# Kernel tuning notes

Hardware: AMD Instinct MI355X
Metric: run time of the kernel (lower is better)

## Reference

```python
import jax, jax.numpy as jnp
import numpy as np

D_MODEL = 2048
D_INNER = 4096            # expand * d_model
D_XB = 1024
D_STATE = 128
HEADDIM = 64
NHEADS = D_INNER // HEADDIM            # 64
NGROUPS = D_INNER // D_STATE           # 32 (d_inner == ngroups * d_state)
HPG = NHEADS // NGROUPS                # heads per B/C group = 2
REPEAT = D_INNER // D_XB               # repeat_kv factor = 4
XB_GROUPS = D_XB // D_STATE            # 8
CHUNK = 256
D_CONV = 4
CONV_DIM = D_INNER + 2 * D_XB          # 6144
D_IN_PROJ = D_INNER + 2 * D_XB + D_INNER + NHEADS  # 10304 -> d_mlp = 0
NORM_GS = D_INNER // NGROUPS           # gated group-RMSNorm group size = 128
EPS = 1e-5


def setup_inputs() -> dict:
    key = jax.random.key(0)
    ks = jax.random.split(key, 8)
    u = jax.random.normal(ks[0], (2, 2048, D_MODEL), jnp.float32)
    W_in = jax.random.normal(ks[1], (D_IN_PROJ, D_MODEL), jnp.float32) * 0.02
    conv_w = jax.random.normal(ks[2], (CONV_DIM, D_CONV), jnp.float32) * 0.2
    conv_b = jnp.zeros((CONV_DIM,), jnp.float32)
    # dt_bias = inverse-softplus of dt ~ LogUniform(dt_min, dt_max), as in __init__
    dt = jnp.exp(jax.random.uniform(ks[3], (NHEADS,), jnp.float32)
                 * (np.log(0.1) - np.log(0.001)) + np.log(0.001))
    dt_bias = dt + jnp.log(-jnp.expm1(-dt))
    A_log = jnp.log(jax.random.uniform(ks[4], (NHEADS,), jnp.float32, minval=1.0, maxval=16.0))
    D = jnp.ones((NHEADS,), jnp.float32)
    norm_weight = jnp.ones((D_INNER,), jnp.float32)
    W_out = jax.random.normal(ks[5], (D_MODEL, D_INNER), jnp.float32) * 0.02
    return dict(u=u, W_in=W_in, conv_w=conv_w, conv_b=conv_b, dt_bias=dt_bias,
                A_log=A_log, D=D, norm_weight=norm_weight, W_out=W_out)


def _segsum(x):
    # x: (..., T); out[..., t, s] = sum_{s < i <= t} x_i for s <= t else -inf
    T = x.shape[-1]
    cs = jnp.cumsum(x, axis=-1)
    seg = cs[..., :, None] - cs[..., None, :]
    mask = jnp.tril(jnp.ones((T, T), bool))
    return jnp.where(mask, seg, -jnp.inf)


def _chunked_scan(x, dt, A, Bh, Ch, D):
    # SSD chunked selective scan (mamba_chunk_scan_combined math).
    # x: (b,l,h,p), dt: (b,l,h) post-softplus, A: (h,), Bh/Ch: (b,l,h,n), D: (h,)
    b, l, h, p = x.shape
    c = l // CHUNK
    xc = x.reshape(b, c, CHUNK, h, p)
    dtc = dt.reshape(b, c, CHUNK, h)
    Bc = Bh.reshape(b, c, CHUNK, h, D_STATE)
    Cc = Ch.reshape(b, c, CHUNK, h, D_STATE)
    dA = jnp.transpose(dtc * A, (0, 3, 1, 2))          # (b,h,c,cl)
    dA_cs = jnp.cumsum(dA, axis=-1)                     # (b,h,c,cl)
    L = jnp.exp(_segsum(dA))                            # (b,h,c,cl,cl), lower-tri decay
    xdt = xc * dtc[..., None]                           # (b,c,cl,h,p)
    # intra-chunk (diagonal block) output
    G = jnp.einsum('bclhn,bcshn->bhcls', Cc, Bc)
    Y_diag = jnp.einsum('bhcls,bcshp->bclhp', G * L, xdt)
    # per-chunk final states
    decay_states = jnp.exp(dA_cs[..., -1:] - dA_cs)     # (b,h,c,cl)
    states = jnp.einsum('bcshn,bhcs,bcshp->bchpn', Bc, decay_states, xdt)
    # inter-chunk recurrence
    chunk_decay = jnp.exp(dA_cs[..., -1])               # (b,h,c)
    states_t = jnp.moveaxis(states, 1, 0)               # (c,b,h,p,n)
    decay_t = jnp.moveaxis(chunk_decay, -1, 0)          # (c,b,h)
    def step(carry, inp):
        s, d = inp
        return carry * d[..., None, None] + s, carry
    _, prev = jax.lax.scan(step, jnp.zeros_like(states_t[0]), (states_t, decay_t))
    prev = jnp.moveaxis(prev, 0, 1)                     # (b,c,h,p,n) state entering each chunk
    Y_off = jnp.einsum('bclhn,bchpn,bhcl->bclhp', Cc, prev, jnp.exp(dA_cs))
    y = Y_diag + Y_off + xc * D[:, None]                # D skip uses raw x
    return y.reshape(b, l, h, p)


def reference(u, W_in, conv_w, conv_b, dt_bias, A_log, D, norm_weight, W_out):
    b, l, _ = u.shape
    zxbcdt = u @ W_in.T                                 # (b,l,10304); d_mlp == 0
    z, xBC, dt = jnp.split(zxbcdt, [D_INNER, D_INNER + CONV_DIM], axis=-1)
    # causal depthwise conv1d (kernel D_CONV) + SiLU (causal_conv1d_fn semantics)
    xp = jnp.pad(xBC, ((0, 0), (D_CONV - 1, 0), (0, 0)))
    conv = conv_b
    for k in range(D_CONV):
        conv = conv + xp[:, k:k + l, :] * conv_w[:, k]
    xBC = jax.nn.silu(conv)
    x, B, C = jnp.split(xBC, [D_XB, 2 * D_XB], axis=-1)
    # GQA-style repeat_kv (repeat_interleave over d_state-sized groups)
    x = jnp.repeat(x.reshape(b, l, XB_GROUPS, D_STATE), REPEAT, axis=2).reshape(b, l, D_INNER)
    B = jnp.repeat(B.reshape(b, l, XB_GROUPS, D_STATE), REPEAT, axis=2)   # (b,l,NGROUPS,n)
    C = C.reshape(b, l, NGROUPS, D_STATE)
    # broadcast groups to heads (head h uses group h // HPG)
    Bh = jnp.repeat(B, HPG, axis=2)
    Ch = jnp.repeat(C, HPG, axis=2)
    xh = x.reshape(b, l, NHEADS, HEADDIM)
    dt = jax.nn.softplus(dt + dt_bias)                  # dt_softplus=True
    A = -jnp.exp(A_log)
    y = _chunked_scan(xh, dt, A, Bh, Ch, D).reshape(b, l, D_INNER)
    # RMSNormGated (norm_before_gate=False): gate then grouped RMSNorm
    y = y * jax.nn.silu(z)
    yg = y.reshape(b, l, NGROUPS, NORM_GS)
    rstd = jax.lax.rsqrt(jnp.mean(yg * yg, axis=-1, keepdims=True) + EPS)
    y = (yg * rstd).reshape(b, l, D_INNER) * norm_weight
    return y @ W_out.T
```

## Files before the change

### kernel.cpp

```cpp
#include <hip/hip_runtime.h>
#include <cstdint>
#include <cstddef>

typedef unsigned int uint;
typedef unsigned short ushort;

typedef __bf16 bf16x8 __attribute__((ext_vector_type(8)));
typedef float f32x4 __attribute__((ext_vector_type(4)));

__device__ __forceinline__ float bflo(uint u) { return __uint_as_float(u << 16); }
__device__ __forceinline__ float bfhi(uint u) { return __uint_as_float(u & 0xffff0000u); }
__device__ __forceinline__ float bf2f(ushort s) { return __uint_as_float(((uint)s) << 16); }
__device__ __forceinline__ ushort f2bf(float f) {
    uint u = __float_as_uint(f);
    u += 0x7fffu + ((u >> 16) & 1u);
    return (ushort)(u >> 16);
}
__device__ __forceinline__ uint pk2(float lo, float hi) {
    return (uint)f2bf(lo) | ((uint)f2bf(hi) << 16);
}
__device__ __forceinline__ void unpack8(uint4 v, float* f) {
    f[0] = bflo(v.x); f[1] = bfhi(v.x); f[2] = bflo(v.y); f[3] = bfhi(v.y);
    f[4] = bflo(v.z); f[5] = bfhi(v.z); f[6] = bflo(v.w); f[7] = bfhi(v.w);
}

typedef __attribute__((address_space(1))) const unsigned int* as1_cuptr;
typedef __attribute__((address_space(3))) unsigned int* as3_uptr;
__device__ __forceinline__ void gload_lds16(const void* g, void* l) {
    __builtin_amdgcn_global_load_lds((as1_cuptr)g, (as3_uptr)l, 16, 0, 0);
}

#define LTOT 4096
#define DMODEL 2048
#define DINNER 4096
#define DSTATE 128
#define NHEADS 64
#define CONVDIM 6144
#define DPROJ 10304
#define CHUNK 256
#define NCHUNK 16

__global__ void cvt_kernel(const float* __restrict__ in, ushort* __restrict__ out, int n4) {
    int i = blockIdx.x * 256 + threadIdx.x;
    if (i < n4) {
        float4 v = ((const float4*)in)[i];
        ushort4 o;
        o.x = f2bf(v.x); o.y = f2bf(v.y); o.z = f2bf(v.z); o.w = f2bf(v.w);
        ((ushort4*)out)[i] = o;
    }
}

#define MFMA_OP __builtin_amdgcn_mfma_f32_16x16x32_bf16
#define MM16(MB) do { \
  acc[(MB)+0][0]=MFMA_OP(a0,b0,acc[(MB)+0][0],0,0,0); acc[(MB)+0][1]=MFMA_OP(a0,b1,acc[(MB)+0][1],0,0,0); \
  acc[(MB)+0][2]=MFMA_OP(a0,b2,acc[(MB)+0][2],0,0,0); acc[(MB)+0][3]=MFMA_OP(a0,b3,acc[(MB)+0][3],0,0,0); \
  acc[(MB)+1][0]=MFMA_OP(a1,b0,acc[(MB)+1][0],0,0,0); acc[(MB)+1][1]=MFMA_OP(a1,b1,acc[(MB)+1][1],0,0,0); \
  acc[(MB)+1][2]=MFMA_OP(a1,b2,acc[(MB)+1][2],0,0,0); acc[(MB)+1][3]=MFMA_OP(a1,b3,acc[(MB)+1][3],0,0,0); \
  acc[(MB)+2][0]=MFMA_OP(a2,b0,acc[(MB)+2][0],0,0,0); acc[(MB)+2][1]=MFMA_OP(a2,b1,acc[(MB)+2][1],0,0,0); \
  acc[(MB)+2][2]=MFMA_OP(a2,b2,acc[(MB)+2][2],0,0,0); acc[(MB)+2][3]=MFMA_OP(a2,b3,acc[(MB)+2][3],0,0,0); \
  acc[(MB)+3][0]=MFMA_OP(a3,b0,acc[(MB)+3][0],0,0,0); acc[(MB)+3][1]=MFMA_OP(a3,b1,acc[(MB)+3][1],0,0,0); \
  acc[(MB)+3][2]=MFMA_OP(a3,b2,acc[(MB)+3][2],0,0,0); acc[(MB)+3][3]=MFMA_OP(a3,b3,acc[(MB)+3][3],0,0,0); \
} while (0)

#define RD8(BASE, OFF) (*(const bf16x8*)((BASE) + (OFF)))

__global__ __launch_bounds__(512, 2) void gemm256_in(
    const ushort* __restrict__ X, const ushort* __restrict__ W,
    ushort* __restrict__ zbuf, ushort* __restrict__ xbc, float* __restrict__ dtraw) {
    __shared__ ushort AL[2][16384];
    __shared__ ushort BL[2][16384];
    const int NBN = 41;
    int q = gridDim.x >> 3;
    int wg = blockIdx.x;
    int swz = (wg & 7) * q + (wg >> 3);
    int per = NBN * 4;
    int sg = swz / per, rr = swz % per;
    int bm = sg * 4 + (rr & 3);
    int bn = rr >> 2;
    int tid = threadIdx.x;
    int lane = tid & 63, w = tid >> 6;
    int wr = w >> 2, wc = w & 3;
    int lr = lane & 15, g = lane >> 4;
    int y00 = ((lr >> 1) << 7) | ((lr & 1) << 6) | (g << 4);
    int z00 = y00 ^ (((y00 >> 7) & 7) << 4);
    int aBase = wr * 8192 + z00;
    int bBase = wc * 4096 + z00;
    int z0 = tid * 16, z1 = z0 + 8192;
    int y0 = z0 ^ (((z0 >> 7) & 7) << 4);
    int y1 = z1 ^ (((z1 >> 7) & 7) << 4);
    int row0s = ((y0 >> 7) << 1) | ((y0 >> 6) & 1), kbe0 = (y0 & 63) >> 1;
    int row1s = ((y1 >> 7) << 1) | ((y1 >> 6) & 1), kbe1 = (y1 & 63) >> 1;
    const ushort* gA0 = &X[(size_t)(bm * 256 + row0s) * 2048 + kbe0];
    const ushort* gA1 = &X[(size_t)(bm * 256 + row1s) * 2048 + kbe1];
    const ushort* gB0 = &W[(size_t)(bn * 256 + row0s) * 2048 + kbe0];
    const ushort* gB1 = &W[(size_t)(bn * 256 + row1s) * 2048 + kbe1];
    int wOff = w * 1024;

#define STAGE(DB, ARR, KP, P0, P1, KO) do { \
    gload_lds16((P0) + (KO) + (KP) * 32, (char*)(ARR) + (DB) * 32768 + (KP) * 16384 + wOff); \
    gload_lds16((P1) + (KO) + (KP) * 32, (char*)(ARR) + (DB) * 32768 + (KP) * 16384 + wOff + 8192); \
} while (0)

    f32x4 acc[8][4] = {};
    STAGE(0, AL, 0, gA0, gA1, 0);
    STAGE(0, BL, 0, gB0, gB1, 0);
    STAGE(0, AL, 1, gA0, gA1, 0);
    STAGE(0, BL, 1, gB0, gB1, 0);

    for (int t = 0; t < 32; ++t) {
        int buf = t & 1, nb = buf ^ 1;
        int ko = ((t + 1) & 31) * 64;
        const char* Ab = (const char*)AL + buf * 32768;
        const char* Bb = (const char*)BL + buf * 32768;
        bf16x8 a0, a1, a2, a3, b0, b1, b2, b3;
        asm volatile("s_waitcnt vmcnt(4)" ::: "memory");
        __builtin_amdgcn_s_barrier();
        __builtin_amdgcn_sched_barrier(0);
        b0 = RD8(Bb, bBase);        b1 = RD8(Bb, bBase + 1024);
        b2 = RD8(Bb, bBase + 2048); b3 = RD8(Bb, bBase + 3072);
        a0 = RD8(Ab, aBase);        a1 = RD8(Ab, aBase + 1024);
        a2 = RD8(Ab, aBase + 2048); a3 = RD8(Ab, aBase + 3072);
        STAGE(nb, AL, 0, gA0, gA1, ko);
        __builtin_amdgcn_s_setprio(1);
        MM16(0);
        __builtin_amdgcn_s_setprio(0);
        __builtin_amdgcn_sched_barrier(0);
        __builtin_amdgcn_s_barrier();
        __builtin_amdgcn_sched_barrier(0);
        a0 = RD8(Ab, aBase + 4096);        a1 = RD8(Ab, aBase + 4096 + 1024);
        a2 = RD8(Ab, aBase + 4096 + 2048); a3 = RD8(Ab, aBase + 4096 + 3072);
        STAGE(nb, BL, 0, gB0, gB1, ko);
        __builtin_amdgcn_s_setprio(1);
        MM16(4);
        __builtin_amdgcn_s_setprio(0);
        asm volatile("s_waitcnt vmcnt(4)" ::: "memory");
        __builtin_amdgcn_s_barrier();
        __builtin_amdgcn_sched_barrier(0);
        b0 = RD8(Bb, bBase + 16384);        b1 = RD8(Bb, bBase + 16384 + 1024);
        b2 = RD8(Bb, bBase + 16384 + 2048); b3 = RD8(Bb, bBase + 16384 + 3072);
        a0 = RD8(Ab, aBase + 16384);        a1 = RD8(Ab, aBase + 16384 + 1024);
        a2 = RD8(Ab, aBase + 16384 + 2048); a3 = RD8(Ab, aBase + 16384 + 3072);
        STAGE(nb, AL, 1, gA0, gA1, ko);
        __builtin_amdgcn_s_setprio(1);
        MM16(0);
        __builtin_amdgcn_s_setprio(0);
        __builtin_amdgcn_sched_barrier(0);
        __builtin_amdgcn_s_barrier();
        __builtin_amdgcn_sched_barrier(0);
        a0 = RD8(Ab, aBase + 16384 + 4096);        a1 = RD8(Ab, aBase + 16384 + 4096 + 1024);
        a2 = RD8(Ab, aBase + 16384 + 4096 + 2048); a3 = RD8(Ab, aBase + 16384 + 4096 + 3072);
        STAGE(nb, BL, 1, gB0, gB1, ko);
        __builtin_amdgcn_s_setprio(1);
        MM16(4);
        __builtin_amdgcn_s_setprio(0);
    }
    asm volatile("s_waitcnt vmcnt(0)" ::: "memory");

    int rq = g * 4;
    #pragma unroll
    for (int mf = 0; mf < 8; mf++) {
        int row0 = bm * 256 + wr * 128 + mf * 16 + rq;
        #pragma unroll
        for (int n = 0; n < 4; n++) {
            int cb0 = bn * 256 + wc * 64 + n * 16;
            int col = cb0 + lr;
            if (cb0 < 4096) {
                #pragma unroll
                for (int r = 0; r < 4; r++)
                    zbuf[(size_t)(row0 + r) * DINNER + col] = f2bf(acc[mf][n][r]);
            } else if (cb0 < 10240) {
                #pragma unroll
                for (int r = 0; r < 4; r++)
                    xbc[(size_t)(row0 + r) * CONVDIM + (col - 4096)] = f2bf(acc[mf][n][r]);
            } else if (cb0 < 10304) {
                #pragma unroll
                for (int r = 0; r < 4; r++)
                    dtraw[(size_t)(row0 + r) * 64 + (col - 10240)] = acc[mf][n][r];
            }
        }
    }
}
#undef STAGE

__global__ __launch_bounds__(512, 2) void gemm256_out(
    const ushort* __restrict__ X, const ushort* __restrict__ W,
    float* __restrict__ outF) {
    __shared__ ushort AL[2][16384];
    __shared__ ushort BL[2][8192];
    int q = gridDim.x >> 3;
    int wg = blockIdx.x;
    int swz = (wg & 7) * q + (wg >> 3);
    int per = 16 * 4;
    int sg = swz / per, rr = swz % per;
    int bm = sg * 4 + (rr & 3);
    int bn = rr >> 2;
    int tid = threadIdx.x;
    int lane = tid & 63, w = tid >> 6;
    int wr = w >> 1, wc = w & 1;
    int lr = lane & 15, g = lane >> 4;
    int y00 = ((lr >> 1) << 7) | ((lr & 1) << 6) | (g << 4);
    int z00 = y00 ^ (((y00 >> 7) & 7) << 4);
    int aBase = wr * 4096 + z00;
    int bBase = wc * 4096 + z00;
    int z0 = tid * 16, z1 = z0 + 8192;
    int y0 = z0 ^ (((z0 >> 7) & 7) << 4);
    int y1 = z1 ^ (((z1 >> 7) & 7) << 4);
    int rowA0 = ((y0 >> 7) << 1) | ((y0 >> 6) & 1), kA0 = (y0 & 63) >> 1;
    int rowA1 = ((y1 >> 7) << 1) | ((y1 >> 6) & 1), kA1 = (y1 & 63) >> 1;
    const ushort* gA0 = &X[(size_t)(bm * 256 + rowA0) * 4096 + kA0];
    const ushort* gA1 = &X[(size_t)(bm * 256 + rowA1) * 4096 + kA1];
    const ushort* gB  = &W[(size_t)(bn * 128 + rowA0) * 4096 + kA0];
    int wOff = w * 1024;

#define STAGEA(DB, KP, KO) do { \
    gload_lds16(gA0 + (KO) + (KP) * 32, (char*)AL + (DB) * 32768 + (KP) * 16384 + wOff); \
    gload_lds16(gA1 + (KO) + (KP) * 32, (char*)AL + (DB) * 32768 + (KP) * 16384 + wOff + 8192); \
} while (0)
#define STAGEB(DB, KP, KO) \
    gload_lds16(gB + (KO) + (KP) * 32, (char*)BL + (DB) * 16384 + (KP) * 8192 + wOff)

    f32x4 acc[4][4] = {};
    STAGEA(0, 0, 0); STAGEB(0, 0, 0);
    STAGEA(0, 1, 0); STAGEB(0, 1, 0);

    for (int t = 0; t < 64; ++t) {
        int buf = t & 1, nb = buf ^ 1;
        int ko = ((t + 1) & 63) * 64;
        const char* Ab = (const char*)AL + buf * 32768;
        const char* Bb = (const char*)BL + buf * 16384;
        bf16x8 a0, a1, a2, a3, b0, b1, b2, b3;
        asm volatile("s_waitcnt vmcnt(3)" ::: "memory");
        __builtin_amdgcn_s_barrier();
        __builtin_amdgcn_sched_barrier(0);
        b0 = RD8(Bb, bBase);        b1 = RD8(Bb, bBase + 1024);
        b2 = RD8(Bb, bBase + 2048); b3 = RD8(Bb, bBase + 3072);
        a0 = RD8(Ab, aBase);        a1 = RD8(Ab, aBase + 1024);
        a2 = RD8(Ab, aBase + 2048); a3 = RD8(Ab, aBase + 3072);
        STAGEA(nb, 0, ko); STAGEB(nb, 0, ko);
        __builtin_amdgcn_s_setprio(1);
        MM16(0);
        __builtin_amdgcn_s_setprio(0);
        __builtin_amdgcn_sched_barrier(0);
        asm volatile("s_waitcnt vmcnt(3)" ::: "memory");
        __builtin_amdgcn_s_barrier();
        __builtin_amdgcn_sched_barrier(0);
        b0 = RD8(Bb, bBase + 8192);        b1 = RD8(Bb, bBase + 8192 + 1024);
        b2 = RD8(Bb, bBase + 8192 + 2048); b3 = RD8(Bb, bBase + 8192 + 3072);
        a0 = RD8(Ab, aBase + 16384);        a1 = RD8(Ab, aBase + 16384 + 1024);
        a2 = RD8(Ab, aBase + 16384 + 2048); a3 = RD8(Ab, aBase + 16384 + 3072);
        STAGEA(nb, 1, ko); STAGEB(nb, 1, ko);
        __builtin_amdgcn_s_setprio(1);
        MM16(0);
        __builtin_amdgcn_s_setprio(0);
        __builtin_amdgcn_sched_barrier(0);
    }
    asm volatile("s_waitcnt vmcnt(0)" ::: "memory");

    int rq = g * 4;
    #pragma unroll
    for (int mf = 0; mf < 4; mf++) {
        int row0 = bm * 256 + wr * 64 + mf * 16 + rq;
        #pragma unroll
        for (int nf = 0; nf < 4; nf++) {
            int col = bn * 128 + wc * 64 + nf * 16 + lr;
            #pragma unroll
            for (int r = 0; r < 4; r++)
                outF[(size_t)(row0 + r) * DMODEL + col] = acc[mf][nf][r];
        }
    }
}
#undef STAGEA
#undef STAGEB

__global__ void conv_kernel(const ushort* __restrict__ xbc, const float* __restrict__ cw,
                            const float* __restrict__ cb, ushort* __restrict__ convout) {
    int c8 = (blockIdx.x * 256 + threadIdx.x) * 8;
    int row0 = blockIdx.y * 4;
    int t0 = row0 & 2047;
    float bias[8];
    {
        float4 b0 = ((const float4*)cb)[c8 / 4];
        float4 b1 = ((const float4*)cb)[c8 / 4 + 1];
        bias[0] = b0.x; bias[1] = b0.y; bias[2] = b0.z; bias[3] = b0.w;
        bias[4] = b1.x; bias[5] = b1.y; bias[6] = b1.z; bias[7] = b1.w;
    }
    float wk[8][4];
    #pragma unroll
    for (int e = 0; e < 8; e++) {
        float4 wv = ((const float4*)cw)[c8 + e];
        wk[e][0] = wv.x; wk[e][1] = wv.y; wk[e][2] = wv.z; wk[e][3] = wv.w;
    }
    float f[7][8];
    #pragma unroll
    for (int j = 0; j < 7; j++) {
        int tt = t0 - 3 + j;
        if (tt >= 0) {
            uint4 v = *(const uint4*)&xbc[(size_t)(row0 - 3 + j) * CONVDIM + c8];
            unpack8(v, f[j]);
        } else {
            #pragma unroll
            for (int e = 0; e < 8; e++) f[j][e] = 0.f;
        }
    }
    #pragma unroll
    for (int r = 0; r < 4; r++) {
        float a[8];
        #pragma unroll
        for (int e = 0; e < 8; e++) {
            a[e] = bias[e];
            #pragma unroll
            for (int k = 0; k < 4; k++) a[e] += f[r + k][e] * wk[e][k];
        }
        uint4 o;
        float s[8];
        #pragma unroll
        for (int e = 0; e < 8; e++) s[e] = a[e] / (1.f + __expf(-a[e]));
        o.x = pk2(s[0], s[1]); o.y = pk2(s[2], s[3]);
        o.z = pk2(s[4], s[5]); o.w = pk2(s[6], s[7]);
        *(uint4*)&convout[(size_t)(row0 + r) * CONVDIM + c8] = o;
    }
}

__global__ void cumsum_kernel(float* __restrict__ dtbuf, const float* __restrict__ dt_bias,
                              const float* __restrict__ A_log, float* __restrict__ dAcs) {
    int bi = blockIdx.x;
    int h = bi & 63, cg = bi >> 6;
    int t = threadIdx.x;
    size_t didx = (size_t)(cg * 256 + t) * 64 + h;
    float x = dtbuf[didx] + dt_bias[h];
    float sp = (x > 20.f) ? x : log1pf(__expf(x));
    dtbuf[didx] = sp;
    float A = -expf(A_log[h]);
    float v = sp * A;
    __shared__ float s[256];
    s[t] = v;
    __syncthreads();
    for (int off = 1; off < 256; off <<= 1) {
        float add = (t >= off) ? s[t - off] : 0.f;
        __syncthreads();
        s[t] += add;
        __syncthreads();
    }
    dAcs[(size_t)bi * 256 + t] = s[t];
}

__global__ __launch_bounds__(256) void states_mfma(
    const ushort* __restrict__ convout, const float* __restrict__ dtsp,
    const float* __restrict__ dAcs, float* __restrict__ states) {
    __shared__ ushort BT[128 * 72];
    __shared__ ushort XT[64 * 72];
    int bi = blockIdx.x;
    int h = bi & 63, cg = bi >> 6;
    int tid = threadIdx.x;
    int rowbase = cg * 256;
    int bcol = 1024 + ((h >> 3) << 7);
    int xcol = ((h >> 3) << 7) + ((h & 1) << 6);
    float dAlast = dAcs[(size_t)bi * 256 + 255];
    int w = tid >> 6, lane = tid & 63, g = lane >> 4, cc = lane & 15;
    f32x4 acc[4][2] = {};
    for (int T = 0; T < 4; T++) {
        __syncthreads();
        int s = lane;
        int srow = rowbase + T * 64 + s;
        #pragma unroll
        for (int i = 0; i < 4; i++) {
            int n0 = (w + i * 4) * 8;
            uint4 v = *(const uint4*)&convout[(size_t)srow * CONVDIM + bcol + n0];
            ushort us[8];
            us[0] = (ushort)v.x; us[1] = (ushort)(v.x >> 16);
            us[2] = (ushort)v.y; us[3] = (ushort)(v.y >> 16);
            us[4] = (ushort)v.z; us[5] = (ushort)(v.z >> 16);
            us[6] = (ushort)v.w; us[7] = (ushort)(v.w >> 16);
            #pragma unroll
            for (int e = 0; e < 8; e++) BT[(n0 + e) * 72 + s] = us[e];
        }
        float wgt = dtsp[(size_t)srow * 64 + h] * __expf(dAlast - dAcs[(size_t)bi * 256 + T * 64 + s]);
        #pragma unroll
        for (int j = 0; j < 2; j++) {
            int p0 = (w * 2 + j) * 8;
            uint4 v = *(const uint4*)&convout[(size_t)srow * CONVDIM + xcol + p0];
            float f[8]; unpack8(v, f);
            #pragma unroll
            for (int e = 0; e < 8; e++) XT[(p0 + e) * 72 + s] = f2bf(f[e] * wgt);
        }
        __syncthreads();
        bf16x8 af[4][2], bw[2][2];
        #pragma unroll
        for (int m = 0; m < 4; m++)
            #pragma unroll
            for (int kb = 0; kb < 2; kb++)
                af[m][kb] = *(const bf16x8*)&XT[(m * 16 + cc) * 72 + kb * 32 + 8 * g];
        #pragma unroll
        for (int np = 0; np < 2; np++)
            #pragma unroll
            for (int kb = 0; kb < 2; kb++)
                bw[np][kb] = *(const bf16x8*)&BT[(w * 32 + np * 16 + cc) * 72 + kb * 32 + 8 * g];
        #pragma unroll
        for (int m = 0; m < 4; m++)
            #pragma unroll
            for (int np = 0; np < 2; np++) {
                acc[m][np] = MFMA_OP(af[m][0], bw[np][0], acc[m][np], 0, 0, 0);
                acc[m][np] = MFMA_OP(af[m][1], bw[np][1], acc[m][np], 0, 0, 0);
            }
    }
    size_t base = (size_t)bi * 8192;
    #pragma unroll
    for (int m = 0; m < 4; m++)
        #pragma unroll
        for (int np = 0; np < 2; np++)
            #pragma unroll
            for (int r = 0; r < 4; r++) {
                int p = m * 16 + 4 * g + r;
                int n = w * 32 + np * 16 + cc;
                states[base + (size_t)p * 128 + n] = acc[m][np][r];
            }
}

__global__ void recur_kernel(const float* __restrict__ dAcs, float* __restrict__ states) {
    int blk = blockIdx.x;
    int pq = blk & 7, bh = blk >> 3;
    int h = bh & 63, b = bh >> 6;
    int tid = threadIdx.x;
    int p = pq * 8 + (tid >> 5);
    int n0 = (tid & 31) * 4;
    float4 carry = make_float4(0.f, 0.f, 0.f, 0.f);
    for (int c = 0; c < 8; c++) {
        int bi = (b * 8 + c) * 64 + h;
        float decay = __expf(dAcs[(size_t)bi * 256 + 255]);
        size_t idx = (size_t)bi * 8192 + (size_t)p * 128 + n0;
        float4 tmp = *(const float4*)&states[idx];
        *(float4*)&states[idx] = carry;
        carry.x = carry.x * decay + tmp.x;
        carry.y = carry.y * decay + tmp.y;
        carry.z = carry.z * decay + tmp.z;
        carry.w = carry.w * decay + tmp.w;
    }
}

__global__ __launch_bounds__(256, 2) void yscan_mfma(
    const ushort* __restrict__ convout, const float* __restrict__ dtsp,
    const float* __restrict__ dAcs, const float* __restrict__ states,
    ushort* __restrict__ y) {
    __shared__ ushort XT[64 * 264];
    __shared__ ushort PR[64 * 136];
    __shared__ ushort PV[4 * 16 * 72];
    __shared__ float sdA[256];
    int bi = blockIdx.x;
    int h = bi & 63, cg = bi >> 6;
    int tid = threadIdx.x;
    int rowbase = cg * 256;
    int bcol = 1024 + ((h >> 3) << 7);
    int ccol = 2048 + ((h >> 1) << 7);
    int xcol = ((h >> 3) << 7) + ((h & 1) << 6);

    sdA[tid] = dAcs[(size_t)bi * 256 + tid];
    #pragma unroll
    for (int i = 0; i < 4; i++) {
        int s = i * 64 + (tid & 63);
        float dtv = dtsp[(size_t)(rowbase + s) * 64 + h];
        #pragma unroll
        for (int j = 0; j < 2; j++) {
            int p0 = (((tid >> 6) << 1) + j) << 3;
            uint4 v = *(const uint4*)&convout[(size_t)(rowbase + s) * CONVDIM + xcol + p0];
            float f[8]; unpack8(v, f);
            #pragma unroll
            for (int e = 0; e < 8; e++) XT[(p0 + e) * 264 + s] = f2bf(f[e] * dtv);
        }
    }
    {
        const float* pv = &states[(size_t)bi * 8192];
        #pragma unroll
        for (int i = 0; i < 8; i++) {
            int flat = i * 1024 + tid * 4;
            float4 v = *(const float4*)&pv[flat];
            int p = flat >> 7, n = flat & 127;
            *(uint*)&PR[p * 136 + n]     = pk2(v.x, v.y);
            *(uint*)&PR[p * 136 + n + 2] = pk2(v.z, v.w);
        }
    }
    __syncthreads();

    int w = tid >> 6, lane = tid & 63, g = lane >> 4, c = lane & 15;
    int wbase = w * 64;
    const ushort* Crow0 = &convout[(size_t)(rowbase + wbase + c) * CONVDIM + ccol + 8 * g];

    f32x4 yac[4][4] = {};
    #pragma unroll
    for (int kb = 0; kb < 4; kb++) {
        bf16x8 pb[4];
        #pragma unroll
        for (int np = 0; np < 4; np++)
            pb[np] = *(const bf16x8*)&PR[(16 * np + c) * 136 + kb * 32 + 8 * g];
        #pragma unroll
        for (int m = 0; m < 4; m++) {
            bf16x8 cf = *(const bf16x8*)&Crow0[(size_t)(m * 16) * CONVDIM + kb * 32];
            #pragma unroll
            for (int np = 0; np < 4; np++)
                yac[m][np] = MFMA_OP(cf, pb[np], yac[m][np], 0, 0, 0);
        }
    }
    float al[4][4];
    float Sw = sdA[wbase];
    float eSw = __expf(Sw);
    #pragma unroll
    for (int m = 0; m < 4; m++)
        #pragma unroll
        for (int r = 0; r < 4; r++) {
            float dAl = sdA[wbase + m * 16 + 4 * g + r];
            al[m][r] = __expf(dAl - Sw);
            float el = al[m][r] * eSw;
            #pragma unroll
            for (int np = 0; np < 4; np++) yac[m][np][r] *= el;
        }

    ushort* pvs = &PV[w * 1152];
    for (int T = 0; T <= w; T++) {
        f32x4 sac[4][4] = {};
        #pragma unroll
        for (int kb = 0; kb < 4; kb++) {
            bf16x8 bb[4];
            #pragma unroll
            for (int np = 0; np < 4; np++)
                bb[np] = *(const bf16x8*)&convout[(size_t)(rowbase + T * 64 + 16 * np + c) * CONVDIM + bcol + kb * 32 + 8 * g];
            #pragma unroll
            for (int m = 0; m < 4; m++) {
                bf16x8 cf = *(const bf16x8*)&Crow0[(size_t)(m * 16) * CONVDIM + kb * 32];
                #pragma unroll
                for (int np = 0; np < 4; np++)
                    sac[m][np] = MFMA_OP(cf, bb[np], sac[m][np], 0, 0, 0);
            }
        }
        bf16x8 xb[4][2];
        #pragma unroll
        for (int np = 0; np < 4; np++)
            #pragma unroll
            for (int k2 = 0; k2 < 2; k2++)
                xb[np][k2] = *(const bf16x8*)&XT[(16 * np + c) * 264 + T * 64 + k2 * 32 + 8 * g];
        if (T < w) {
            float ET = sdA[T * 64 + 63];
            float cT = __expf(Sw - ET);
            float bc[4];
            #pragma unroll
            for (int np = 0; np < 4; np++)
                bc[np] = __expf(ET - sdA[T * 64 + 16 * np + c]) * cT;
            #pragma unroll
            for (int m = 0; m < 4; m++) {
                #pragma unroll
                for (int np = 0; np < 4; np++) {
                    float s0 = bc[np];
                    #pragma unroll
                    for (int r = 0; r < 4; r++)
                        pvs[(4 * g + r) * 72 + 16 * np + c] = f2bf(sac[m][np][r] * (al[m][r] * s0));
                }
                bf16x8 pa0 = *(const bf16x8*)&pvs[c * 72 + 8 * g];
                bf16x8 pa1 = *(const bf16x8*)&pvs[c * 72 + 32 + 8 * g];
                #pragma unroll
                for (int np = 0; np < 4; np++) {
                    yac[m][np] = MFMA_OP(pa0, xb[np][0], yac[m][np], 0, 0, 0);
                    yac[m][np] = MFMA_OP(pa1, xb[np][1], yac[m][np], 0, 0, 0);
                }
            }
        } else {
            #pragma unroll
            for (int m = 0; m < 4; m++) {
                float dal[4];
                #pragma unroll
                for (int r = 0; r < 4; r++) dal[r] = sdA[wbase + m * 16 + 4 * g + r];
                #pragma unroll
                for (int np = 0; np < 4; np++) {
                    int s_loc = w * 64 + 16 * np + c;
                    float dAs = sdA[s_loc];
                    #pragma unroll
                    for (int r = 0; r < 4; r++) {
                        int l_loc = wbase + m * 16 + 4 * g + r;
                        float v = (s_loc <= l_loc) ? sac[m][np][r] * __expf(dal[r] - dAs) : 0.f;
                        pvs[(4 * g + r) * 72 + 16 * np + c] = f2bf(v);
                    }
                }
                bf16x8 pa0 = *(const bf16x8*)&pvs[c * 72 + 8 * g];
                bf16x8 pa1 = *(const bf16x8*)&pvs[c * 72 + 32 + 8 * g];
                #pragma unroll
                for (int np = 0; np < 4; np++) {
                    yac[m][np] = MFMA_OP(pa0, xb[np][0], yac[m][np], 0, 0, 0);
                    yac[m][np] = MFMA_OP(pa1, xb[np][1], yac[m][np], 0, 0, 0);
                }
            }
        }
    }
    #pragma unroll
    for (int m = 0; m < 4; m++)
        #pragma unroll
        for (int np = 0; np < 4; np++)
            #pragma unroll
            for (int r = 0; r < 4; r++) {
                int l = wbase + m * 16 + 4 * g + r;
                y[(size_t)(rowbase + l) * DINNER + h * 64 + 16 * np + c] = f2bf(yac[m][np][r]);
            }
}

__global__ void norm_kernel(ushort* __restrict__ y, const ushort* __restrict__ zbuf,
                            const ushort* __restrict__ convout, const float* __restrict__ Dvec,
                            const float* __restrict__ nw) {
    int row = blockIdx.x;
    int g = blockIdx.y * 4 + (threadIdx.x >> 6);
    int lane = threadIdx.x & 63;
    int cbase = g * 128 + lane * 2;
    int h = cbase >> 6;
    int p = cbase & 63;
    int xc = ((h >> 3) << 7) + ((h & 1) << 6) + p;
    uint yv = *(const uint*)&y[(size_t)row * DINNER + cbase];
    uint zv = *(const uint*)&zbuf[(size_t)row * DINNER + cbase];
    uint xv = *(const uint*)&convout[(size_t)row * CONVDIM + xc];
    float Dh = Dvec[h];
    float y0 = bflo(yv) + Dh * bflo(xv), y1 = bfhi(yv) + Dh * bfhi(xv);
    float z0 = bflo(zv), z1 = bfhi(zv);
    float v0 = y0 * (z0 / (1.f + __expf(-z0)));
    float v1 = y1 * (z1 / (1.f + __expf(-z1)));
    float ss = v0 * v0 + v1 * v1;
    #pragma unroll
    for (int off = 32; off; off >>= 1) ss += __shfl_xor(ss, off, 64);
    float rstd = rsqrtf(ss * (1.f / 128.f) + 1e-5f);
    v0 *= rstd * nw[cbase];
    v1 *= rstd * nw[cbase + 1];
    *(uint*)&y[(size_t)row * DINNER + cbase] = pk2(v0, v1);
}

extern "C" void kernel_launch(void* const* d_in, const int* in_sizes, int n_in,
                              void* d_out, int out_size, void* d_ws, size_t ws_size,
                              hipStream_t stream) {
    const float* u       = (const float*)d_in[0];
    const float* W_in    = (const float*)d_in[1];
    const float* conv_w  = (const float*)d_in[2];
    const float* conv_b  = (const float*)d_in[3];
    const float* dt_bias = (const float*)d_in[4];
    const float* A_log   = (const float*)d_in[5];
    const float* Dvec    = (const float*)d_in[6];
    const float* nw      = (const float*)d_in[7];
    const float* W_out   = (const float*)d_in[8];

    char* ws = (char*)d_ws;
    size_t off = 0;
    auto alloc = [&](size_t bytes) { void* p = ws + off; off += (bytes + 255) & ~(size_t)255; return p; };
    ushort* zbuf    = (ushort*)alloc((size_t)LTOT * DINNER * 2);
    void*   shreg   = alloc((size_t)LTOT * CONVDIM * 2);
    ushort* xbc     = (ushort*)shreg;
    float*  states  = (float*)shreg;
    ushort* Wout_bf = (ushort*)shreg;
    float*  dtbuf   = (float*) alloc((size_t)LTOT * 64 * 4);
    void*   convreg = alloc((size_t)LTOT * CONVDIM * 2);
    ushort* Win_bf  = (ushort*)convreg;
    ushort* convout = (ushort*)convreg;
    float*  dAcs    = (float*) alloc((size_t)1024 * 256 * 4);
    void*   ybreg   = alloc((size_t)LTOT * DINNER * 2);
    ushort* u_bf    = (ushort*)ybreg;
    ushort* ybuf    = (ushort*)ybreg;

    cvt_kernel<<<dim3(8192),  dim3(256), 0, stream>>>(u, u_bf, 2097152);
    cvt_kernel<<<dim3(20608), dim3(256), 0, stream>>>(W_in, Win_bf, 5275648);
    gemm256_in<<<dim3(656), dim3(512), 0, stream>>>(u_bf, Win_bf, zbuf, xbc, dtbuf);
    conv_kernel<<<dim3(3, 1024), dim3(256), 0, stream>>>(xbc, conv_w, conv_b, convout);
    cumsum_kernel<<<dim3(1024), dim3(256), 0, stream>>>(dtbuf, dt_bias, A_log, dAcs);
    states_mfma<<<dim3(1024), dim3(256), 0, stream>>>(convout, dtbuf, dAcs, states);
    recur_kernel<<<dim3(1024), dim3(256), 0, stream>>>(dAcs, states);
    yscan_mfma<<<dim3(1024), dim3(256), 0, stream>>>(convout, dtbuf, dAcs, states, ybuf);
    cvt_kernel<<<dim3(8192), dim3(256), 0, stream>>>(W_out, Wout_bf, 2097152);
    norm_kernel<<<dim3(4096, 8), dim3(256), 0, stream>>>(ybuf, zbuf, convout, Dvec, nw);
    gemm256_out<<<dim3(256), dim3(512), 0, stream>>>(ybuf, Wout_bf, (float*)d_out);
}
```

Baseline: 498.7 us.

## Software-pipeline LDS fragment reads in input-projection GEMM across MFMA phases

Restructures the in-projection GEMM main loop so each phase's LDS fragment loads for the next phase are issued before the current phase's MFMAs run. The fragments are kept in separate register arrays, and the first k-half of the next buffer is prefetched at the end of each iteration. This cuts the number of barriers per iteration from four to two and retunes the vmcnt waits, aiming to hide LDS latency behind matrix math. The cost is more live vector registers, which could cause spills under the 2-block occupancy bound, plus subtler synchronization correctness around buffer reuse.

```diff
diff --git a/kernel.cpp b/kernel.cpp
--- a/kernel.cpp
+++ b/kernel.cpp
@@ -51,15 +51,12 @@
 }
 
 #define MFMA_OP __builtin_amdgcn_mfma_f32_16x16x32_bf16
-#define MM16(MB) do { \
-  acc[(MB)+0][0]=MFMA_OP(a0,b0,acc[(MB)+0][0],0,0,0); acc[(MB)+0][1]=MFMA_OP(a0,b1,acc[(MB)+0][1],0,0,0); \
-  acc[(MB)+0][2]=MFMA_OP(a0,b2,acc[(MB)+0][2],0,0,0); acc[(MB)+0][3]=MFMA_OP(a0,b3,acc[(MB)+0][3],0,0,0); \
-  acc[(MB)+1][0]=MFMA_OP(a1,b0,acc[(MB)+1][0],0,0,0); acc[(MB)+1][1]=MFMA_OP(a1,b1,acc[(MB)+1][1],0,0,0); \
-  acc[(MB)+1][2]=MFMA_OP(a1,b2,acc[(MB)+1][2],0,0,0); acc[(MB)+1][3]=MFMA_OP(a1,b3,acc[(MB)+1][3],0,0,0); \
-  acc[(MB)+2][0]=MFMA_OP(a2,b0,acc[(MB)+2][0],0,0,0); acc[(MB)+2][1]=MFMA_OP(a2,b1,acc[(MB)+2][1],0,0,0); \
-  acc[(MB)+2][2]=MFMA_OP(a2,b2,acc[(MB)+2][2],0,0,0); acc[(MB)+2][3]=MFMA_OP(a2,b3,acc[(MB)+2][3],0,0,0); \
-  acc[(MB)+3][0]=MFMA_OP(a3,b0,acc[(MB)+3][0],0,0,0); acc[(MB)+3][1]=MFMA_OP(a3,b1,acc[(MB)+3][1],0,0,0); \
-  acc[(MB)+3][2]=MFMA_OP(a3,b2,acc[(MB)+3][2],0,0,0); acc[(MB)+3][3]=MFMA_OP(a3,b3,acc[(MB)+3][3],0,0,0); \
+#define MMX(MB, AV, BV) do { \
+  _Pragma("unroll") \
+  for (int _m = 0; _m < 4; _m++) \
+    _Pragma("unroll") \
+    for (int _n = 0; _n < 4; _n++) \
+      acc[(MB)+_m][_n] = MFMA_OP(AV[_m], BV[_n], acc[(MB)+_m][_n], 0, 0, 0); \
 } while (0)
 
 #define RD8(BASE, OFF) (*(const bf16x8*)((BASE) + (OFF)))
@@ -102,57 +99,71 @@
 } while (0)
 
     f32x4 acc[8][4] = {};
+    bf16x8 bLo[4], bHi[4], aE[4], aO[4];
     STAGE(0, AL, 0, gA0, gA1, 0);
     STAGE(0, BL, 0, gB0, gB1, 0);
     STAGE(0, AL, 1, gA0, gA1, 0);
     STAGE(0, BL, 1, gB0, gB1, 0);
+    asm volatile("s_waitcnt vmcnt(4)" ::: "memory");
+    __builtin_amdgcn_s_barrier();
+    __builtin_amdgcn_sched_barrier(0);
+    {
+        const char* Ab = (const char*)AL;
+        const char* Bb = (const char*)BL;
+        #pragma unroll
+        for (int i = 0; i < 4; i++) {
+            bLo[i] = RD8(Bb, bBase + i * 1024);
+            aE[i]  = RD8(Ab, aBase + i * 1024);
+        }
+    }
 
     for (int t = 0; t < 32; ++t) {
         int buf = t & 1, nb = buf ^ 1;
         int ko = ((t + 1) & 31) * 64;
-        const char* Ab = (const char*)AL + buf * 32768;
-        const char* Bb = (const char*)BL + buf * 32768;
-        bf16x8 a0, a1, a2, a3, b0, b1, b2, b3;
-        asm volatile("s_waitcnt vmcnt(4)" ::: "memory");
-        __builtin_amdgcn_s_barrier();
-        __builtin_amdgcn_sched_barrier(0);
-        b0 = RD8(Bb, bBase);        b1 = RD8(Bb, bBase + 1024);
-        b2 = RD8(Bb, bBase + 2048); b3 = RD8(Bb, bBase + 3072);
-        a0 = RD8(Ab, aBase);        a1 = RD8(Ab, aBase + 1024);
-        a2 = RD8(Ab, aBase + 2048); a3 = RD8(Ab, aBase + 3072);
+        const char* Ab  = (const char*)AL + buf * 32768;
+        const char* Bb  = (const char*)BL + buf * 32768;
+        const char* AbN = (const char*)AL + nb * 32768;
+        const char* BbN = (const char*)BL + nb * 32768;
+        #pragma unroll
+        for (int i = 0; i < 4; i++) aO[i] = RD8(Ab, aBase + 4096 + i * 1024);
         STAGE(nb, AL, 0, gA0, gA1, ko);
         __builtin_amdgcn_s_setprio(1);
-        MM16(0);
+        MMX(0, aE, bLo);
         __builtin_amdgcn_s_setprio(0);
         __builtin_amdgcn_sched_barrier(0);
+        asm volatile("s_waitcnt vmcnt(2)" ::: "memory");
         __builtin_amdgcn_s_barrier();
         __builtin_amdgcn_sched_barrier(0);
-        a0 = RD8(Ab, aBase + 4096);        a1 = RD8(Ab, aBase + 4096 + 1024);
-        a2 = RD8(Ab, aBase + 4096 + 2048); a3 = RD8(Ab, aBase + 4096 + 3072);
+        #pragma unroll
+        for (int i = 0; i < 4; i++) {
+            bHi[i] = RD8(Bb, bBase + 16384 + i * 1024);
+            aE[i]  = RD8(Ab, aBase + 16384 + i * 1024);
+        }
         STAGE(nb, BL, 0, gB0, gB1, ko);
         __builtin_amdgcn_s_setprio(1);
-        MM16(4);
+        MMX(4, aO, bLo);
         __builtin_amdgcn_s_setprio(0);
-        asm volatile("s_waitcnt vmcnt(4)" ::: "memory");
-        __builtin_amdgcn_s_barrier();
-        __builtin_amdgcn_sched_barrier(0);
-        b0 = RD8(Bb, bBase + 16384);        b1 = RD8(Bb, bBase + 16384 + 1024);
-        b2 = RD8(Bb, bBase + 16384 + 2048); b3 = RD8(Bb, bBase + 16384 + 3072);
-        a0 = RD8(Ab, aBase + 16384);        a1 = RD8(Ab, aBase + 16384 + 1024);
-        a2 = RD8(Ab, aBase + 16384 + 2048); a3 = RD8(Ab, aBase + 16384 + 3072);
+        __builtin_amdgcn_sched_barrier(0);
+        #pragma unroll
+        for (int i = 0; i < 4; i++) aO[i] = RD8(Ab, aBase + 16384 + 4096 + i * 1024);
         STAGE(nb, AL, 1, gA0, gA1, ko);
         __builtin_amdgcn_s_setprio(1);
-        MM16(0);
+        MMX(0, aE, bHi);
         __builtin_amdgcn_s_setprio(0);
         __builtin_amdgcn_sched_barrier(0);
+        asm volatile("s_waitcnt vmcnt(2)" ::: "memory");
         __builtin_amdgcn_s_barrier();
         __builtin_amdgcn_sched_barrier(0);
-        a0 = RD8(Ab, aBase + 16384 + 4096);        a1 = RD8(Ab, aBase + 16384 + 4096 + 1024);
-        a2 = RD8(Ab, aBase + 16384 + 4096 + 2048); a3 = RD8(Ab, aBase + 16384 + 4096 + 3072);
+        #pragma unroll
+        for (int i = 0; i < 4; i++) {
+            bLo[i] = RD8(BbN, bBase + i * 1024);
+            aE[i]  = RD8(AbN, aBase + i * 1024);
+        }
         STAGE(nb, BL, 1, gB0, gB1, ko);
         __builtin_amdgcn_s_setprio(1);
-        MM16(4);
+        MMX(4, aO, bHi);
         __builtin_amdgcn_s_setprio(0);
+        __builtin_amdgcn_sched_barrier(0);
     }
     asm volatile("s_waitcnt vmcnt(0)" ::: "memory");
 
@@ -181,6 +192,17 @@
     }
 }
 #undef STAGE
+
+#define MM16(MB) do { \
+  acc[(MB)+0][0]=MFMA_OP(a0,b0,acc[(MB)+0][0],0,0,0); acc[(MB)+0][1]=MFMA_OP(a0,b1,acc[(MB)+0][1],0,0,0); \
+  acc[(MB)+0][2]=MFMA_OP(a0,b2,acc[(MB)+0][2],0,0,0); acc[(MB)+0][3]=MFMA_OP(a0,b3,acc[(MB)+0][3],0,0,0); \
+  acc[(MB)+1][0]=MFMA_OP(a1,b0,acc[(MB)+1][0],0,0,0); acc[(MB)+1][1]=MFMA_OP(a1,b1,acc[(MB)+1][1],0,0,0); \
+  acc[(MB)+1][2]=MFMA_OP(a1,b2,acc[(MB)+1][2],0,0,0); acc[(MB)+1][3]=MFMA_OP(a1,b3,acc[(MB)+1][3],0,0,0); \
+  acc[(MB)+2][0]=MFMA_OP(a2,b0,acc[(MB)+2][0],0,0,0); acc[(MB)+2][1]=MFMA_OP(a2,b1,acc[(MB)+2][1],0,0,0); \
+  acc[(MB)+2][2]=MFMA_OP(a2,b2,acc[(MB)+2][2],0,0,0); acc[(MB)+2][3]=MFMA_OP(a2,b3,acc[(MB)+2][3],0,0,0); \
+  acc[(MB)+3][0]=MFMA_OP(a3,b0,acc[(MB)+3][0],0,0,0); acc[(MB)+3][1]=MFMA_OP(a3,b1,acc[(MB)+3][1],0,0,0); \
+  acc[(MB)+3][2]=MFMA_OP(a3,b2,acc[(MB)+3][2],0,0,0); acc[(MB)+3][3]=MFMA_OP(a3,b3,acc[(MB)+3][3],0,0,0); \
+} while (0)
 
 __global__ __launch_bounds__(512, 2) void gemm256_out(
     const ushort* __restrict__ X, const ushort* __restrict__ W,
```

New measurement: 468.2 us. -6.1%, faster.
